# Performance work log

Hardware: AMD Instinct MI355X
Metric: run time of the kernel (lower is better)

## Reference

```python
import jax, jax.numpy as jnp
import numpy as np

NUM_HEADS = 32
ROPE_BASE = 10000.0


def _rotate_half(x):
    h = x.shape[-1] // 2
    return jnp.concatenate([-x[..., h:], x[..., :h]], axis=-1)


def setup_inputs() -> dict:
    key = jax.random.key(0)
    ks = jax.random.split(key, 6)
    B, S, H = 2, 2048, 4096
    hidden_states = jax.random.normal(ks[0], (B, S, H), dtype=jnp.float32)
    # additive causal mask: 0 on/below diagonal, large negative above
    causal = jnp.tril(jnp.ones((S, S), dtype=bool))
    attention_mask = jnp.where(causal, 0.0, -1e9).astype(jnp.float32)
    attention_mask = jnp.broadcast_to(attention_mask[None, None], (B, 1, S, S))
    position_ids = jnp.broadcast_to(jnp.arange(S, dtype=jnp.int64 if jax.config.jax_enable_x64 else jnp.int32)[None, :], (B, S))
    scale = 1.0 / np.sqrt(H)
    Wq = jax.random.normal(ks[1], (H, H), dtype=jnp.float32) * scale
    Wk = jax.random.normal(ks[2], (H, H), dtype=jnp.float32) * scale
    Wv = jax.random.normal(ks[3], (H, H), dtype=jnp.float32) * scale
    Wo = jax.random.normal(ks[4], (H, H), dtype=jnp.float32) * scale
    return {"hidden_states": hidden_states, "attention_mask": attention_mask,
            "position_ids": position_ids, "Wq": Wq, "Wk": Wk, "Wv": Wv, "Wo": Wo}


def reference(hidden_states, attention_mask, position_ids, Wq, Wk, Wv, Wo):
    B, S, H = hidden_states.shape
    nh = NUM_HEADS
    hd = H // nh
    # QKV projections (torch Linear: y = x @ W.T), split heads -> [B, nh, S, hd]
    def proj(W):
        y = jnp.einsum('bsh,oh->bso', hidden_states, W)
        return y.reshape(B, S, nh, hd).transpose(0, 2, 1, 3)
    q, k, v = proj(Wq), proj(Wk), proj(Wv)
    # rotary embeddings gathered at position_ids
    inv_freq = 1.0 / (ROPE_BASE ** (jnp.arange(0, hd, 2, dtype=jnp.float32) / hd))
    freqs = position_ids.astype(jnp.float32)[:, :, None] * inv_freq[None, None, :]  # [B,S,hd/2]
    emb = jnp.concatenate([freqs, freqs], axis=-1)  # [B,S,hd]
    cos = jnp.cos(emb)[:, None, :, :]  # [B,1,S,hd]
    sin = jnp.sin(emb)[:, None, :, :]
    q = q * cos + _rotate_half(q) * sin
    k = k * cos + _rotate_half(k) * sin
    # scaled dot-product attention
    scores = jnp.einsum('bhqd,bhkd->bhqk', q, k) / jnp.sqrt(jnp.float32(hd))
    scores = scores + attention_mask
    scores = jnp.maximum(scores, jnp.finfo(scores.dtype).min)
    attn = jax.nn.softmax(scores, axis=-1)
    out = jnp.einsum('bhqk,bhkd->bhqd', attn, v)  # [B,nh,S,hd]
    out = out.transpose(0, 2, 1, 3).reshape(B, S, H)
    return jnp.einsum('bsh,oh->bso', out, Wo)
```

## Files before the change

kernel.cpp:

```cpp
#include <hip/hip_runtime.h>
#include <cstdint>
#include <cmath>

typedef __bf16 bf16;
typedef __bf16 bf16x8 __attribute__((ext_vector_type(8)));
typedef __bf16 bf16x4 __attribute__((ext_vector_type(4)));
typedef float f32x4 __attribute__((ext_vector_type(4)));

#define B_ 2
#define S_ 2048
#define H_ 4096
#define NH 32
#define HD 128

#define VMCNT(n) asm volatile("s_waitcnt vmcnt(" #n ")" ::: "memory")
#define BAR() __builtin_amdgcn_s_barrier()

__device__ __forceinline__ void gl_lds16(const void* g, void* l) {
  __builtin_amdgcn_global_load_lds(
      (const __attribute__((address_space(1))) unsigned int*)g,
      (__attribute__((address_space(3))) unsigned int*)l, 16, 0, 0);
}

__global__ __launch_bounds__(256) void cast_kernel(const float* __restrict__ in,
                                                   bf16* __restrict__ out, int n4) {
  int i = blockIdx.x * 256 + threadIdx.x;
  if (i < n4) {
    float4 v = ((const float4*)in)[i];
    bf16x4 o = {(bf16)v.x, (bf16)v.y, (bf16)v.z, (bf16)v.w};
    ((bf16x4*)out)[i] = o;
  }
}

template <int TM, int TN>
__device__ __forceinline__ void mfma_q(f32x4 (&acc)[8][4], bf16x8 (&a)[4][2],
                                       bf16x8 (&b)[2][2]) {
  __builtin_amdgcn_s_setprio(1);
#pragma unroll
  for (int i = 0; i < 4; ++i)
#pragma unroll
    for (int j = 0; j < 2; ++j)
#pragma unroll
      for (int kf = 0; kf < 2; ++kf)
        acc[TM * 4 + i][TN * 2 + j] = __builtin_amdgcn_mfma_f32_16x16x32_bf16(
            a[i][kf], b[j][kf], acc[TM * 4 + i][TN * 2 + j], 0, 0, 0);
  __builtin_amdgcn_s_setprio(0);
}

template <int EPI, int NC>
__global__ __launch_bounds__(512, 2) void gemm256(const bf16* __restrict__ A,
                                                  const bf16* __restrict__ B0g,
                                                  const bf16* __restrict__ B1g,
                                                  const bf16* __restrict__ B2g,
                                                  void* __restrict__ C0g,
                                                  void* __restrict__ C1g,
                                                  void* __restrict__ C2g) {
  constexpr int K = 4096, N = 4096, KT = K / 64;
  __shared__ __attribute__((aligned(16))) char lds[131072];
  char* Al = lds;
  char* Bl = lds + 65536;
  int tid = threadIdx.x;
  int l = tid & 63, lr = l & 15, lg = l >> 4;
  int w = tid >> 6, wm = w >> 2, wn = w & 3;
  int bid = (int)blockIdx.x;
  int x = bid & 7, local = bid >> 3;
  int lr0b = local / NC, lc0 = local % NC;
  int r0 = (x * 2 + lr0b) * 256;
  int g = lc0 >> 4;
  int c0 = (lc0 & 15) * 256;
  const bf16* Bw = (g == 0) ? B0g : ((g == 1) ? B1g : B2g);
  const bf16* Ab = A + (size_t)r0 * K;
  const bf16* Bb = Bw + (size_t)c0 * K;

  int lr0 = tid >> 3;
  int cel = (((tid & 7) ^ ((tid >> 3) & 7)) << 3);

  auto stageA = [&](int buf, int mh, int k0) {
    char* dst = Al + buf * 32768 + mh * 16384 + tid * 16;
    int ra = mh * 64 + lr0;
    gl_lds16(Ab + (size_t)ra * K + k0 + cel, dst);
    gl_lds16(Ab + (size_t)(ra + 128) * K + k0 + cel, dst + 8192);
  };
  auto stageB = [&](int buf, int nh, int k0) {
    char* dst = Bl + buf * 32768 + nh * 16384 + tid * 16;
    int n0 = (lr0 >> 5) * 64 + nh * 32 + (lr0 & 31);
    gl_lds16(Bb + (size_t)n0 * K + k0 + cel, dst);
    gl_lds16(Bb + (size_t)(n0 + 128) * K + k0 + cel, dst + 8192);
  };

  int rsw = (lr & 7) << 4;
  auto ldA = [&](bf16x8 (&dst)[4][2], int buf, int mh) {
    char* base = Al + buf * 32768 + mh * 16384 + wm * 8192;
#pragma unroll
    for (int mfl = 0; mfl < 4; ++mfl)
#pragma unroll
      for (int kf = 0; kf < 2; ++kf)
        __builtin_memcpy(&dst[mfl][kf],
                         base + (mfl * 16 + lr) * 128 + ((kf * 64 + lg * 16) ^ rsw), 16);
  };
  auto ldB = [&](bf16x8 (&dst)[2][2], int buf, int nh) {
    char* base = Bl + buf * 32768 + nh * 16384 + wn * 4096;
#pragma unroll
    for (int nfl = 0; nfl < 2; ++nfl)
#pragma unroll
      for (int kf = 0; kf < 2; ++kf)
        __builtin_memcpy(&dst[nfl][kf],
                         base + (nfl * 16 + lr) * 128 + ((kf * 64 + lg * 16) ^ rsw), 16);
  };

  bf16x8 af[4][2], bf0[2][2], bf1[2][2];
  f32x4 acc[8][4] = {};

  stageA(0, 0, 0);
  stageB(0, 0, 0);
  stageB(0, 1, 0);
  stageA(0, 1, 0);
  VMCNT(4); BAR();

  for (int kt = 0; kt < KT - 1; ++kt) {
    int buf = kt & 1, nb = buf ^ 1;
    int k0n = (kt + 1) * 64;
    ldA(af, buf, 0);
    ldB(bf0, buf, 0);
    stageA(nb, 0, k0n);
    stageB(nb, 0, k0n);
    mfma_q<0, 0>(acc, af, bf0);
    VMCNT(4); BAR();
    ldB(bf1, buf, 1);
    stageB(nb, 1, k0n);
    mfma_q<0, 1>(acc, af, bf1);
    ldA(af, buf, 1);
    stageA(nb, 1, k0n);
    mfma_q<1, 1>(acc, af, bf1);
    mfma_q<1, 0>(acc, af, bf0);
    VMCNT(4); BAR();
  }
  {
    int buf = (KT - 1) & 1;
    ldA(af, buf, 0);
    ldB(bf0, buf, 0);
    mfma_q<0, 0>(acc, af, bf0);
    VMCNT(2); BAR();
    ldB(bf1, buf, 1);
    mfma_q<0, 1>(acc, af, bf1);
    VMCNT(0); BAR();
    ldA(af, buf, 1);
    mfma_q<1, 1>(acc, af, bf1);
    mfma_q<1, 0>(acc, af, bf0);
  }

  void* Cg = (g == 0) ? C0g : ((g == 1) ? C1g : C2g);
#pragma unroll
  for (int mf = 0; mf < 8; ++mf)
#pragma unroll
    for (int nf = 0; nf < 4; ++nf) {
      int orow = r0 + wm * 128 + mf * 16 + lg * 4;
      int ocol = c0 + wn * 64 + nf * 16 + lr;
      if (EPI == 0) {
        bf16* C = (bf16*)Cg;
#pragma unroll
        for (int jr = 0; jr < 4; ++jr)
          C[(size_t)(orow + jr) * N + ocol] = (bf16)acc[mf][nf][jr];
      } else {
        float* C = (float*)Cg;
#pragma unroll
        for (int jr = 0; jr < 4; ++jr)
          C[(size_t)(orow + jr) * N + ocol] = acc[mf][nf][jr];
      }
    }
}

__global__ __launch_bounds__(256) void rope_kernel(bf16* __restrict__ Qx,
                                                   bf16* __restrict__ Kx,
                                                   const int* __restrict__ pos,
                                                   float qscale) {
  int r = blockIdx.x;
  bf16* X = blockIdx.y ? Kx : Qx;
  float scale = blockIdx.y ? 1.0f : qscale;
  float pf = (float)pos[r];
  int i = threadIdx.x & 63;
  int h0 = threadIdx.x >> 6;
  float ang = pf * exp2f(-0.20762050593046868f * (float)i);
  float sn = sinf(ang), cs = cosf(ang);
  bf16* row = X + (size_t)r * H_;
#pragma unroll
  for (int h = h0; h < NH; h += 4) {
    bf16* p = row + h * HD + i;
    float a = (float)p[0], b = (float)p[64];
    p[0] = (bf16)((a * cs - b * sn) * scale);
    p[64] = (bf16)((b * cs + a * sn) * scale);
  }
}

__global__ __launch_bounds__(256) void transpose_v(const bf16* __restrict__ V,
                                                   bf16* __restrict__ Vt) {
  __shared__ __attribute__((aligned(16))) bf16 tile[64][130];
  int bh = blockIdx.y;
  int b = bh >> 5, h = bh & 31;
  int s0 = blockIdx.x * 64;
  int t = threadIdx.x;
  const bf16* src = V + (size_t)(b * S_ + s0) * H_ + h * HD;
  int rr = t >> 4, cc = (t & 15) * 8;
#pragma unroll
  for (int k = 0; k < 4; ++k) {
    bf16x8 v;
    __builtin_memcpy(&v, src + (size_t)(rr + k * 16) * H_ + cc, 16);
#pragma unroll
    for (int u = 0; u < 8; ++u) tile[rr + k * 16][cc + u] = v[u];
  }
  __syncthreads();
  bf16* dst = Vt + (size_t)bh * HD * S_;
  int sl = t & 63, d0 = t >> 6;
  for (int j = 0; j < 32; ++j) {
    int d = d0 + j * 4;
    dst[(size_t)d * S_ + s0 + sl] = tile[sl][d];
  }
}

__global__ __launch_bounds__(512, 4) void attn_kernel(const bf16* __restrict__ Q,
                                                      const bf16* __restrict__ Km,
                                                      const bf16* __restrict__ Vt,
                                                      bf16* __restrict__ Out) {
  __shared__ __attribute__((aligned(16))) bf16 Ks[2][64 * 128];
  __shared__ __attribute__((aligned(16))) bf16 Vs[2][128 * 64];
  __shared__ __attribute__((aligned(16))) bf16 P_lds[8][16 * 64];
  int tid = threadIdx.x;
  int w = tid >> 6, l = tid & 63;
  int lr = l & 15, lg = l >> 4;
  int f = (int)(blockIdx.y * gridDim.x + blockIdx.x);
  int wk = (f & 7) * 128 + (f >> 3);
  int bh = wk >> 4, b = bh >> 5, h = bh & 31;
  int qt = 15 - (wk & 15);
  int q0w = qt * 128 + w * 16;
  const bf16* Qb = Q + (size_t)b * S_ * H_ + h * HD;
  const char* Kg = (const char*)(Km + (size_t)b * S_ * H_ + h * HD);
  const char* Vg = (const char*)(Vt + (size_t)bh * HD * S_);
  bf16* Ob = Out + (size_t)b * S_ * H_ + h * HD;

  bf16x8 qf[4];
#pragma unroll
  for (int dk = 0; dk < 4; ++dk)
    __builtin_memcpy(&qf[dk], Qb + (size_t)(q0w + lr) * H_ + dk * 32 + lg * 8, 16);

  f32x4 o[8] = {};
  float m = -INFINITY, ls = 0.f;
  int nkv_blk = 2 * qt + 2;
  int nkv_w = 2 * qt + (w >> 2) + 1;

  auto stageK = [&](int buf, int kv0) {
#pragma unroll
    for (int p = 0; p < 2; ++p) {
      int row = p * 32 + (tid >> 4);
      int src = ((tid & 15) * 16) ^ ((row & 7) << 4);
      gl_lds16(Kg + (size_t)(kv0 + row) * (H_ * 2) + src,
               (char*)&Ks[buf][0] + p * 8192 + w * 1024);
    }
  };
  auto stageV = [&](int buf, int kv0) {
#pragma unroll
    for (int p = 0; p < 2; ++p) {
      int row = p * 64 + (tid >> 3);
      int src = ((tid & 7) * 16) ^ ((row & 7) << 4);
      gl_lds16(Vg + (size_t)row * (S_ * 2) + (size_t)kv0 * 2 + src,
               (char*)&Vs[buf][0] + p * 8192 + w * 1024);
    }
  };

  stageK(0, 0);
  stageV(0, 0);
  __syncthreads();

  int cur = 0;
  char* Pl = (char*)&P_lds[w][0];
  for (int t = 0; t < nkv_blk; ++t) {
    int kv0 = t * 64;
    if (t + 1 < nkv_blk) {
      stageK(cur ^ 1, kv0 + 64);
      stageV(cur ^ 1, kv0 + 64);
    }
    if (t < nkv_w) {
      const char* Kl = (const char*)&Ks[cur][0];
      const char* Vl = (const char*)&Vs[cur][0];
      f32x4 s4[4] = {};
      __builtin_amdgcn_s_setprio(1);
#pragma unroll
      for (int dk = 0; dk < 4; ++dk)
#pragma unroll
        for (int st = 0; st < 4; ++st) {
          int row = st * 16 + lr;
          int cb = (dk * 64 + lg * 16) ^ ((row & 7) << 4);
          bf16x8 kf;
          __builtin_memcpy(&kf, Kl + row * 256 + cb, 16);
          s4[st] = __builtin_amdgcn_mfma_f32_16x16x32_bf16(kf, qf[dk], s4[st], 0, 0, 0);
        }
      __builtin_amdgcn_s_setprio(0);
      if (t == nkv_w - 1) {
        int qg = q0w + lr;
#pragma unroll
        for (int st = 0; st < 4; ++st)
#pragma unroll
          for (int j = 0; j < 4; ++j)
            if (kv0 + st * 16 + lg * 4 + j > qg) s4[st][j] = -INFINITY;
      }
      float mx = -INFINITY;
#pragma unroll
      for (int st = 0; st < 4; ++st)
#pragma unroll
        for (int j = 0; j < 4; ++j) mx = fmaxf(mx, s4[st][j]);
      mx = fmaxf(mx, __shfl_xor(mx, 16));
      mx = fmaxf(mx, __shfl_xor(mx, 32));
      float sc = 1.0f;
      if (!__all((int)(mx <= m + 8.0f))) {
        float mn = fmaxf(m, mx);
        sc = exp2f(m - mn);
        m = mn;
        float scq0 = __shfl(sc, lg * 4 + 0);
        float scq1 = __shfl(sc, lg * 4 + 1);
        float scq2 = __shfl(sc, lg * 4 + 2);
        float scq3 = __shfl(sc, lg * 4 + 3);
#pragma unroll
        for (int dt = 0; dt < 8; ++dt) {
          o[dt][0] *= scq0; o[dt][1] *= scq1; o[dt][2] *= scq2; o[dt][3] *= scq3;
        }
      }
      float pv[4][4], rs = 0.f;
#pragma unroll
      for (int st = 0; st < 4; ++st)
#pragma unroll
        for (int j = 0; j < 4; ++j) {
          pv[st][j] = exp2f(s4[st][j] - m);
          rs += pv[st][j];
        }
      ls = ls * sc + rs;
#pragma unroll
      for (int st = 0; st < 4; ++st) {
        bf16x4 pk = {(bf16)pv[st][0], (bf16)pv[st][1], (bf16)pv[st][2], (bf16)pv[st][3]};
        *(bf16x4*)(Pl + lr * 128 + ((st * 32 + lg * 8) ^ ((lr & 7) << 4))) = pk;
      }
      bf16x8 pa[2];
#pragma unroll
      for (int ks = 0; ks < 2; ++ks)
        __builtin_memcpy(&pa[ks], Pl + lr * 128 + ((ks * 64 + lg * 16) ^ ((lr & 7) << 4)), 16);
      __builtin_amdgcn_s_setprio(1);
#pragma unroll
      for (int dt = 0; dt < 8; ++dt)
#pragma unroll
        for (int ks = 0; ks < 2; ++ks) {
          int row = dt * 16 + lr;
          int cb = (ks * 64 + lg * 16) ^ ((row & 7) << 4);
          bf16x8 vf;
          __builtin_memcpy(&vf, Vl + row * 128 + cb, 16);
          o[dt] = __builtin_amdgcn_mfma_f32_16x16x32_bf16(pa[ks], vf, o[dt], 0, 0, 0);
        }
      __builtin_amdgcn_s_setprio(0);
    }
    __syncthreads();
    cur ^= 1;
  }
  ls += __shfl_xor(ls, 16);
  ls += __shfl_xor(ls, 32);
  float lsq[4];
#pragma unroll
  for (int j = 0; j < 4; ++j) lsq[j] = __shfl(ls, lg * 4 + j);
#pragma unroll
  for (int j = 0; j < 4; ++j) {
    float inv = 1.0f / lsq[j];
#pragma unroll
    for (int dt = 0; dt < 8; ++dt)
      Ob[(size_t)(q0w + lg * 4 + j) * H_ + dt * 16 + lr] = (bf16)(o[dt][j] * inv);
  }
}

extern "C" void kernel_launch(void* const* d_in, const int* in_sizes, int n_in,
                              void* d_out, int out_size, void* d_ws, size_t ws_size,
                              hipStream_t stream) {
  const float* X = (const float*)d_in[0];
  const int* pos = (const int*)d_in[2];
  const float* Wq = (const float*)d_in[3];
  const float* Wk = (const float*)d_in[4];
  const float* Wv = (const float*)d_in[5];
  const float* Wo = (const float*)d_in[6];
  float* out = (float*)d_out;
  char* ws = (char*)d_ws;
  const size_t MB32 = 32ull << 20;
  bf16* Xb = (bf16*)ws;
  bf16* Wb = (bf16*)(ws + MB32);
  bf16* Qb = (bf16*)(ws + 2 * MB32);
  bf16* Kb = (bf16*)(ws + 3 * MB32);
  bf16* Vb = (bf16*)(ws + 4 * MB32);
  bf16* Vt = (bf16*)(ws + 5 * MB32);
  bf16* Wvb = (bf16*)d_out;

  const int n4 = (4096 * 4096) / 4;
  dim3 cgrid(n4 / 256), cblk(256);

  cast_kernel<<<cgrid, cblk, 0, stream>>>(X, Xb, n4);
  cast_kernel<<<cgrid, cblk, 0, stream>>>(Wq, Wb, n4);
  cast_kernel<<<cgrid, cblk, 0, stream>>>(Wk, Vt, n4);
  cast_kernel<<<cgrid, cblk, 0, stream>>>(Wv, Wvb, n4);

  gemm256<0, 48><<<dim3(768), dim3(512), 0, stream>>>(Xb, Wb, Vt, Wvb, Qb, Kb, Vb);

  const float qscale = 1.4426950408889634f / 11.313708498984760f;
  rope_kernel<<<dim3(4096, 2), 256, 0, stream>>>(Qb, Kb, pos, qscale);
  transpose_v<<<dim3(32, 64), 256, 0, stream>>>(Vb, Vt);

  attn_kernel<<<dim3(16, 64), 512, 0, stream>>>(Qb, Kb, Vt, Xb);

  cast_kernel<<<cgrid, cblk, 0, stream>>>(Wo, Wb, n4);
  gemm256<1, 16><<<dim3(256), dim3(512), 0, stream>>>(Xb, Wb, Wb, Wb, out, out, out);
}
```

Measured before the change: 762.6 us.

## Double attention Q tile to 256 rows with 1024-thread blocks; batch input casts

```diff
diff --git a/kernel.cpp b/kernel.cpp
--- a/kernel.cpp
+++ b/kernel.cpp
@@ -20,6 +20,25 @@
   __builtin_amdgcn_global_load_lds(
       (const __attribute__((address_space(1))) unsigned int*)g,
       (__attribute__((address_space(3))) unsigned int*)l, 16, 0, 0);
+}
+
+__global__ __launch_bounds__(256) void cast4_kernel(const float* __restrict__ s0,
+                                                    bf16* __restrict__ d0,
+                                                    const float* __restrict__ s1,
+                                                    bf16* __restrict__ d1,
+                                                    const float* __restrict__ s2,
+                                                    bf16* __restrict__ d2,
+                                                    const float* __restrict__ s3,
+                                                    bf16* __restrict__ d3, int n4) {
+  int g = blockIdx.y;
+  const float* in = (g == 0) ? s0 : (g == 1) ? s1 : (g == 2) ? s2 : s3;
+  bf16* out = (g == 0) ? d0 : (g == 1) ? d1 : (g == 2) ? d2 : d3;
+  int i = blockIdx.x * 256 + threadIdx.x;
+  if (i < n4) {
+    float4 v = ((const float4*)in)[i];
+    bf16x4 o = {(bf16)v.x, (bf16)v.y, (bf16)v.z, (bf16)v.w};
+    ((bf16x4*)out)[i] = o;
+  }
 }
 
 __global__ __launch_bounds__(256) void cast_kernel(const float* __restrict__ in,
@@ -217,21 +236,21 @@
   }
 }
 
-__global__ __launch_bounds__(512, 4) void attn_kernel(const bf16* __restrict__ Q,
-                                                      const bf16* __restrict__ Km,
-                                                      const bf16* __restrict__ Vt,
-                                                      bf16* __restrict__ Out) {
+__global__ __launch_bounds__(1024, 4) void attn_kernel(const bf16* __restrict__ Q,
+                                                       const bf16* __restrict__ Km,
+                                                       const bf16* __restrict__ Vt,
+                                                       bf16* __restrict__ Out) {
   __shared__ __attribute__((aligned(16))) bf16 Ks[2][64 * 128];
   __shared__ __attribute__((aligned(16))) bf16 Vs[2][128 * 64];
-  __shared__ __attribute__((aligned(16))) bf16 P_lds[8][16 * 64];
+  __shared__ __attribute__((aligned(16))) bf16 P_lds[16][16 * 64];
   int tid = threadIdx.x;
   int w = tid >> 6, l = tid & 63;
   int lr = l & 15, lg = l >> 4;
   int f = (int)(blockIdx.y * gridDim.x + blockIdx.x);
-  int wk = (f & 7) * 128 + (f >> 3);
-  int bh = wk >> 4, b = bh >> 5, h = bh & 31;
-  int qt = 15 - (wk & 15);
-  int q0w = qt * 128 + w * 16;
+  int wk = (f & 7) * 64 + (f >> 3);
+  int bh = wk >> 3, b = bh >> 5, h = bh & 31;
+  int qt = 7 - (wk & 7);
+  int q0w = qt * 256 + w * 16;
   const bf16* Qb = Q + (size_t)b * S_ * H_ + h * HD;
   const char* Kg = (const char*)(Km + (size_t)b * S_ * H_ + h * HD);
   const char* Vg = (const char*)(Vt + (size_t)bh * HD * S_);
@@ -244,26 +263,19 @@
 
   f32x4 o[8] = {};
   float m = -INFINITY, ls = 0.f;
-  int nkv_blk = 2 * qt + 2;
-  int nkv_w = 2 * qt + (w >> 2) + 1;
+  int nkv_blk = 4 * qt + 4;
+  int nkv_w = 4 * qt + (w >> 2) + 1;
 
   auto stageK = [&](int buf, int kv0) {
-#pragma unroll
-    for (int p = 0; p < 2; ++p) {
-      int row = p * 32 + (tid >> 4);
-      int src = ((tid & 15) * 16) ^ ((row & 7) << 4);
-      gl_lds16(Kg + (size_t)(kv0 + row) * (H_ * 2) + src,
-               (char*)&Ks[buf][0] + p * 8192 + w * 1024);
-    }
+    int row = tid >> 4;
+    int src = ((tid & 15) * 16) ^ ((row & 7) << 4);
+    gl_lds16(Kg + (size_t)(kv0 + row) * (H_ * 2) + src, (char*)&Ks[buf][0] + tid * 16);
   };
   auto stageV = [&](int buf, int kv0) {
-#pragma unroll
-    for (int p = 0; p < 2; ++p) {
-      int row = p * 64 + (tid >> 3);
-      int src = ((tid & 7) * 16) ^ ((row & 7) << 4);
-      gl_lds16(Vg + (size_t)row * (S_ * 2) + (size_t)kv0 * 2 + src,
-               (char*)&Vs[buf][0] + p * 8192 + w * 1024);
-    }
+    int row = tid >> 3;
+    int src = ((tid & 7) * 16) ^ ((row & 7) << 4);
+    gl_lds16(Vg + (size_t)row * (S_ * 2) + (size_t)kv0 * 2 + src,
+             (char*)&Vs[buf][0] + tid * 16);
   };
 
   stageK(0, 0);
@@ -392,12 +404,9 @@
   bf16* Wvb = (bf16*)d_out;
 
   const int n4 = (4096 * 4096) / 4;
-  dim3 cgrid(n4 / 256), cblk(256);
-
-  cast_kernel<<<cgrid, cblk, 0, stream>>>(X, Xb, n4);
-  cast_kernel<<<cgrid, cblk, 0, stream>>>(Wq, Wb, n4);
-  cast_kernel<<<cgrid, cblk, 0, stream>>>(Wk, Vt, n4);
-  cast_kernel<<<cgrid, cblk, 0, stream>>>(Wv, Wvb, n4);
+  dim3 cblk(256);
+
+  cast4_kernel<<<dim3(n4 / 256, 4), cblk, 0, stream>>>(X, Xb, Wq, Wb, Wk, Vt, Wv, Wvb, n4);
 
   gemm256<0, 48><<<dim3(768), dim3(512), 0, stream>>>(Xb, Wb, Vt, Wvb, Qb, Kb, Vb);
 
@@ -405,8 +414,8 @@
   rope_kernel<<<dim3(4096, 2), 256, 0, stream>>>(Qb, Kb, pos, qscale);
   transpose_v<<<dim3(32, 64), 256, 0, stream>>>(Vb, Vt);
 
-  attn_kernel<<<dim3(16, 64), 512, 0, stream>>>(Qb, Kb, Vt, Xb);
-
-  cast_kernel<<<cgrid, cblk, 0, stream>>>(Wo, Wb, n4);
+  attn_kernel<<<dim3(8, 64), 1024, 0, stream>>>(Qb, Kb, Vt, Xb);
+
+  cast_kernel<<<dim3(n4 / 256), cblk, 0, stream>>>(Wo, Wb, n4);
   gemm256<1, 16><<<dim3(256), dim3(512), 0, stream>>>(Xb, Wb, Wb, Wb, out, out, out);
 }
```

Result: slower. 781.1 us (+2.4%).
